# Kernel tuning notes

Hardware: AMD Instinct MI355X
Metric: run time of the kernel (lower is better)

The kernel has to match this reference:

```python
import jax, jax.numpy as jnp
import numpy as np
from jax import lax

B_, L, D, EXPAND, N, R, K = 2, 1024, 1024, 2, 16, 64, 4
ED = EXPAND * D


def setup_inputs() -> dict:
    key = jax.random.key(0)
    ks = jax.random.split(key, 8)
    x = jax.random.normal(ks[0], (B_, L, D), dtype=jnp.float32)
    in_proj_w = jax.random.normal(ks[1], (2 * ED, D), dtype=jnp.float32) * (D ** -0.5)
    in_proj_b = jnp.zeros((2 * ED,), jnp.float32)
    conv_w = jax.random.normal(ks[2], (ED, 1, K), dtype=jnp.float32) * (K ** -0.5)
    conv_b = jnp.zeros((ED,), jnp.float32)
    x_proj_w = jax.random.normal(ks[3], (R + 2 * N, ED), dtype=jnp.float32) * (ED ** -0.5)
    dt_proj_w = jax.random.uniform(ks[4], (ED, R), jnp.float32, -(R ** -0.5), R ** -0.5)
    # inverse-softplus of dt ~ U[log(dt_min), log(dt_max)] (matches torch init)
    dt = jnp.exp(jax.random.uniform(ks[5], (ED,), jnp.float32) * (np.log(0.1) - np.log(0.001)) + np.log(0.001))
    dt_proj_b = dt + jnp.log(-jnp.expm1(-dt))  # softplus^{-1}(dt)
    A_log = jnp.log(jnp.broadcast_to(jnp.arange(1, N + 1, dtype=jnp.float32), (ED, N)))
    D_param = jnp.ones((ED,), jnp.float32)
    out_proj_w = jax.random.normal(ks[6], (D, ED), dtype=jnp.float32) * (ED ** -0.5)
    return {"x": x, "in_proj_w": in_proj_w, "in_proj_b": in_proj_b, "conv_w": conv_w,
            "conv_b": conv_b, "x_proj_w": x_proj_w, "dt_proj_w": dt_proj_w,
            "dt_proj_b": dt_proj_b, "A_log": A_log, "D_param": D_param,
            "out_proj_w": out_proj_w}


def _mamba_fwd(x, in_proj_w, in_proj_b, conv_w, conv_b, x_proj_w, dt_proj_w,
               dt_proj_b, A_log, D_param, out_proj_w):
    xz = x @ in_proj_w.T + in_proj_b                       # (B, L, 2*ED)
    xc, z = jnp.split(xz, 2, axis=-1)                      # (B, L, ED) each
    # causal depthwise conv over time (pad left K-1, valid)
    xc = xc.transpose(0, 2, 1)                             # (B, ED, L)
    xc = lax.conv_general_dilated(xc, conv_w, window_strides=(1,),
                                  padding=[(K - 1, 0)], feature_group_count=ED)
    xc = xc + conv_b[None, :, None]
    xc = jax.nn.silu(xc.transpose(0, 2, 1))                # (B, L, ED)
    # SSM params
    A = -jnp.exp(A_log)                                    # (ED, N)
    dbc = xc @ x_proj_w.T                                  # (B, L, R+2N)
    dt, Bmat, Cmat = jnp.split(dbc, [R, R + N], axis=-1)
    dt = jax.nn.softplus(dt @ dt_proj_w.T + dt_proj_b)     # (B, L, ED)
    dA = jnp.exp(dt[..., None] * A)                        # (B, L, ED, N)
    dBx = (dt * xc)[..., None] * Bmat[:, :, None, :]       # (B, L, ED, N)
    # parallel scan: h_t = dA_t * h_{t-1} + dBx_t
    def combine(e1, e2):
        a1, b1 = e1
        a2, b2 = e2
        return a1 * a2, a2 * b1 + b2
    _, hs = lax.associative_scan(combine, (dA, dBx), axis=1)  # (B, L, ED, N)
    y = jnp.einsum('bln,blen->ble', Cmat, hs) + D_param * xc  # (B, L, ED)
    out = (y * jax.nn.silu(z)) @ out_proj_w.T                 # (B, L, D)
    return out


def reference(x, in_proj_w, in_proj_b, conv_w, conv_b, x_proj_w, dt_proj_w,
              dt_proj_b, A_log, D_param, out_proj_w):
    return _mamba_fwd(x, in_proj_w, in_proj_b, conv_w, conv_b, x_proj_w,
                      dt_proj_w, dt_proj_b, A_log, D_param, out_proj_w)
```

## Files before the change

### kernel.cpp

```cpp
#include <hip/hip_runtime.h>
#include <cstddef>


#define BL   2048
#define DIM  1024
#define ED   2048
#define NST  16
#define RLOW 64
#define CH   64
#define LC   16
#define SK   16
#define DBCN 196608

typedef __attribute__((ext_vector_type(4))) float   f32x4;
typedef __attribute__((ext_vector_type(8))) __bf16  bf16x8;
typedef __attribute__((ext_vector_type(8))) unsigned short us8;

__device__ __forceinline__ float silu_(float x) {
  return x / (1.f + __expf(-x));
}

__device__ __forceinline__ unsigned short f2b(float x) {
  union { float f; unsigned int u; } v; v.f = x;
  unsigned int r = v.u + 0x7FFFu + ((v.u >> 16) & 1u);
  return (unsigned short)(r >> 16);
}

__device__ __forceinline__ float b2f(unsigned short u) {
  union { unsigned int i; float f; } v; v.i = (unsigned int)u << 16; return v.f;
}

__device__ __forceinline__ f32x4 mfma_bf16(us8 a, us8 b, f32x4 c) {
  return __builtin_amdgcn_mfma_f32_16x16x32_bf16(
      __builtin_bit_cast(bf16x8, a), __builtin_bit_cast(bf16x8, b), c, 0, 0, 0);
}

#define GLOAD_LDS16(gaddr, laddr)                                              \
  __builtin_amdgcn_global_load_lds(                                            \
      (const __attribute__((address_space(1))) unsigned int*)(gaddr),          \
      (__attribute__((address_space(3))) unsigned int*)(laddr), 16, 0, 0)

template <int BM, int BN, bool OBF>
__global__ __launch_bounds__(256) void gemm_bf16(
    const unsigned short* __restrict__ A,
    const unsigned short* __restrict__ W,
    const float* __restrict__ bias,
    void* __restrict__ Cp, int ldc, int Nout, int Kloop, int lda, int sstride)
{
  constexpr int BK     = 64;
  constexpr int FM     = BM / 32;
  constexpr int FN     = BN / 32;
  constexpr int NLA    = BM / 32;
  constexpr int NLW    = BN / 32;
  constexpr int ABYTES = BM * BK * 2;
  constexpr int WBYTES = BN * BK * 2;
  __shared__ char smem[2 * (ABYTES + WBYTES)];

  const int tid  = threadIdx.x;
  const int w    = tid >> 6;
  const int lane = tid & 63;
  const int wr   = w >> 1, wc = w & 1;
  const int bm   = blockIdx.x * BM;
  const int bn   = blockIdx.y * BN;
  const int kb   = blockIdx.z * Kloop;

  f32x4 acc[FM][FN];
#pragma unroll
  for (int m = 0; m < FM; ++m)
#pragma unroll
    for (int n = 0; n < FN; ++n) acc[m][n] = (f32x4){0.f, 0.f, 0.f, 0.f};

  const int srow = ((tid >> 7) << 4) | (tid & 15);
  const int kch  = (tid >> 4) & 7;
  const int wofs = (tid >> 6) * 1024;

  const unsigned short* Ag = A + (size_t)(bm + srow) * lda + kb + kch * 8;
  const unsigned short* Wg = W + (size_t)(bn + srow) * lda + kb + kch * 8;

#define STAGE(cur, k0)                                                         \
  {                                                                            \
    char* ab = smem + (cur) * (ABYTES + WBYTES);                               \
    char* wb = ab + ABYTES;                                                    \
    _Pragma("unroll")                                                          \
    for (int j = 0; j < NLA; ++j)                                              \
      GLOAD_LDS16(Ag + (size_t)(j * 32) * lda + (k0), ab + j * 4096 + wofs);   \
    _Pragma("unroll")                                                          \
    for (int j = 0; j < NLW; ++j)                                              \
      GLOAD_LDS16(Wg + (size_t)(j * 32) * lda + (k0), wb + j * 4096 + wofs);   \
  }

  STAGE(0, 0);
  int cur = 0;
  const int NT = Kloop / BK;
  for (int t = 0; t < NT; ++t) {
    __syncthreads();
    if (t + 1 < NT) STAGE(cur ^ 1, (t + 1) * BK);

    const char* ab = smem + cur * (ABYTES + WBYTES);
    const char* wb = ab + ABYTES;
    us8 af[FM][2], wf[FN][2];
#pragma unroll
    for (int m = 0; m < FM; ++m)
#pragma unroll
      for (int h = 0; h < 2; ++h)
        af[m][h] = *(const us8*)(ab + (wr * FM + m) * 2048 + h * 1024 + lane * 16);
#pragma unroll
    for (int n = 0; n < FN; ++n)
#pragma unroll
      for (int h = 0; h < 2; ++h)
        wf[n][h] = *(const us8*)(wb + (wc * FN + n) * 2048 + h * 1024 + lane * 16);
#pragma unroll
    for (int h = 0; h < 2; ++h)
#pragma unroll
      for (int m = 0; m < FM; ++m)
#pragma unroll
        for (int n = 0; n < FN; ++n)
          acc[m][n] = mfma_bf16(af[m][h], wf[n][h], acc[m][n]);
    cur ^= 1;
  }
#undef STAGE

  const int rbase = (lane >> 4) * 4;
  float* Cf = (float*)Cp + (size_t)blockIdx.z * sstride;
#pragma unroll
  for (int m = 0; m < FM; ++m) {
#pragma unroll
    for (int n = 0; n < FN; ++n) {
      const int col = bn + wc * (BN / 2) + n * 16 + (lane & 15);
      if (col < Nout) {
        const float bv = bias ? bias[col] : 0.f;
#pragma unroll
        for (int r = 0; r < 4; ++r) {
          const int row = bm + wr * (BM / 2) + m * 16 + rbase + r;
          const float v = acc[m][n][r] + bv;
          if (OBF) ((unsigned short*)Cp)[(size_t)row * ldc + col] = f2b(v);
          else     Cf[(size_t)row * ldc + col] = v;
        }
      }
    }
  }
}

__global__ __launch_bounds__(256) void reduce_dbc_k(
    const float* __restrict__ par, float* __restrict__ dbc)
{
  const int i = blockIdx.x * 256 + threadIdx.x;
  float4 s = ((const float4*)par)[i];
#pragma unroll
  for (int sk = 1; sk < SK; ++sk) {
    float4 v = ((const float4*)(par + (size_t)sk * DBCN))[i];
    s.x += v.x; s.y += v.y; s.z += v.z; s.w += v.w;
  }
  ((float4*)dbc)[i] = s;
}

__global__ __launch_bounds__(256) void reduce_out_k(
    const float* __restrict__ par, float* __restrict__ out)
{
  const int i = blockIdx.x * 256 + threadIdx.x;
  float4 a = ((const float4*)par)[i];
  float4 b = ((const float4*)(par + 2097152))[i];
  a.x += b.x; a.y += b.y; a.z += b.z; a.w += b.w;
  ((float4*)out)[i] = a;
}

template <int ACT>
__global__ __launch_bounds__(256) void gemm_nt(
    const float* __restrict__ A, int lda,
    const float* __restrict__ W, int ldw,
    const float* __restrict__ bias,
    float* __restrict__ C, int ldc,
    int N, int K)
{
  __shared__ float As[16][64];
  __shared__ float Ws[16][64];
  const int tid = threadIdx.x;
  const int bm = blockIdx.x * 64;
  const int bn = blockIdx.y * 64;
  const int tx = tid & 15;
  const int ty = tid >> 4;
  const int srow = tid >> 2;
  const int scg  = (tid & 3) * 4;

  float acc[4][4] = {};
  const float* Aptr = A + (size_t)(bm + srow) * lda + scg;
  const bool   wok  = (bn + srow) < N;
  const float* Wptr = W + (size_t)(bn + srow) * ldw + scg;

  for (int k0 = 0; k0 < K; k0 += 16) {
    float4 av = *(const float4*)(Aptr + k0);
    float4 wv = make_float4(0.f, 0.f, 0.f, 0.f);
    if (wok) wv = *(const float4*)(Wptr + k0);
    __syncthreads();
    As[scg + 0][srow] = av.x; As[scg + 1][srow] = av.y;
    As[scg + 2][srow] = av.z; As[scg + 3][srow] = av.w;
    Ws[scg + 0][srow] = wv.x; Ws[scg + 1][srow] = wv.y;
    Ws[scg + 2][srow] = wv.z; Ws[scg + 3][srow] = wv.w;
    __syncthreads();
#pragma unroll
    for (int k = 0; k < 16; ++k) {
      float4 a4 = *(const float4*)&As[k][ty * 4];
      float4 w4 = *(const float4*)&Ws[k][tx * 4];
      float a_[4] = {a4.x, a4.y, a4.z, a4.w};
      float w_[4] = {w4.x, w4.y, w4.z, w4.w};
#pragma unroll
      for (int i = 0; i < 4; ++i)
#pragma unroll
        for (int j = 0; j < 4; ++j)
          acc[i][j] += a_[i] * w_[j];
    }
  }

#pragma unroll
  for (int i = 0; i < 4; ++i) {
    const int row = bm + ty * 4 + i;
#pragma unroll
    for (int j = 0; j < 4; ++j) {
      const int col = bn + tx * 4 + j;
      if (col < N) {
        float v = acc[i][j];
        if (bias) v += bias[col];
        if (ACT == 1) v = (v > 20.f) ? v : log1pf(__expf(v));
        C[(size_t)row * ldc + col] = v;
      }
    }
  }
}

__global__ __launch_bounds__(256) void cvt_all_k(
    const float* __restrict__ x, const float* __restrict__ inw,
    const float* __restrict__ ow, const float* __restrict__ xpw,
    unsigned short* __restrict__ xb, unsigned short* __restrict__ iwb,
    unsigned short* __restrict__ owb, unsigned short* __restrict__ xpwb)
{
  const int i = blockIdx.x * 256 + threadIdx.x;
  const float* src; unsigned short* dst; int j;
  if (i < 524288)       { src = x;   dst = xb;  j = i; }
  else if (i < 1572864) { src = inw; dst = iwb; j = i - 524288; }
  else if (i < 2097152) { src = ow;  dst = owb; j = i - 1572864; }
  else {
    j = i - 2097152;
    const int idx = j * 4;
    ushort4 o = {0, 0, 0, 0};
    if ((idx >> 11) < 96) {
      float4 v = *(const float4*)(xpw + idx);
      o.x = f2b(v.x); o.y = f2b(v.y); o.z = f2b(v.z); o.w = f2b(v.w);
    }
    *(ushort4*)(xpwb + idx) = o;
    return;
  }
  float4 v = ((const float4*)src)[j];
  ushort4 o;
  o.x = f2b(v.x); o.y = f2b(v.y); o.z = f2b(v.z); o.w = f2b(v.w);
  ((ushort4*)dst)[j] = o;
}

__global__ __launch_bounds__(256) void conv_silu_k(
    const unsigned short* __restrict__ xzb, const float* __restrict__ cw,
    const float* __restrict__ cb, unsigned short* __restrict__ xcb)
{
  const int idx = blockIdx.x * 256 + threadIdx.x;
  const int row = idx >> 9;
  const int e   = (idx & 511) * 4;
  const int l   = row & 1023;
  const unsigned short* base = xzb + (size_t)(row - l) * (2 * ED) + e;

  float4 cbv = *(const float4*)(cb + e);
  float a0 = cbv.x, a1 = cbv.y, a2 = cbv.z, a3 = cbv.w;
#pragma unroll
  for (int k = 0; k < 4; ++k) {
    const int ls = l - 3 + k;
    if (ls >= 0) {
      ushort4 u = *(const ushort4*)(base + (size_t)ls * (2 * ED));
      a0 += cw[(size_t)(e + 0) * 4 + k] * b2f(u.x);
      a1 += cw[(size_t)(e + 1) * 4 + k] * b2f(u.y);
      a2 += cw[(size_t)(e + 2) * 4 + k] * b2f(u.z);
      a3 += cw[(size_t)(e + 3) * 4 + k] * b2f(u.w);
    }
  }
  ushort4 o;
  o.x = f2b(silu_(a0)); o.y = f2b(silu_(a1));
  o.z = f2b(silu_(a2)); o.w = f2b(silu_(a3));
  *(ushort4*)(xcb + (size_t)row * ED + e) = o;
}

__global__ __launch_bounds__(256, 4) void scan_phase1(
    const float* __restrict__ dt, const unsigned short* __restrict__ xcb,
    const float* __restrict__ dbc, const float* __restrict__ A_log,
    float* __restrict__ aprod_o, float* __restrict__ bfin_o)
{
  const int g  = blockIdx.x * 256 + threadIdx.x;
  const int e  = g & (ED - 1);
  const int bc = g >> 11;
  const int b  = bc >> 6;
  const int c  = bc & (CH - 1);
  const size_t rowbase = (size_t)b * 1024 + (size_t)c * LC;

  __shared__ float4 sB[LC][4];
  if (threadIdx.x < LC * 4) {
    const int row = threadIdx.x >> 2, q = threadIdx.x & 3;
    sB[row][q] = ((const float4*)(dbc + (rowbase + row) * 96 + RLOW))[q];
  }
  __syncthreads();

  float Aen[NST];
  {
    const float4* Ap = (const float4*)(A_log + (size_t)e * NST);
#pragma unroll
    for (int q = 0; q < 4; ++q) {
      float4 v = Ap[q];
      Aen[q*4+0] = -__expf(v.x); Aen[q*4+1] = -__expf(v.y);
      Aen[q*4+2] = -__expf(v.z); Aen[q*4+3] = -__expf(v.w);
    }
  }

  float dtv[LC], dxv[LC];
#pragma unroll
  for (int i = 0; i < LC; ++i) dtv[i] = dt[(rowbase + i) * ED + e];
#pragma unroll
  for (int i = 0; i < LC; ++i)
    dxv[i] = dtv[i] * b2f(xcb[(rowbase + i) * ED + e]);

  float h[NST], ap[NST];
#pragma unroll
  for (int n = 0; n < NST; ++n) { h[n] = 0.f; ap[n] = 1.f; }

  for (int i = 0; i < LC; ++i) {
    float Bv[NST];
#pragma unroll
    for (int q = 0; q < 4; ++q) {
      float4 v = sB[i][q];
      Bv[q*4+0]=v.x; Bv[q*4+1]=v.y; Bv[q*4+2]=v.z; Bv[q*4+3]=v.w;
    }
#pragma unroll
    for (int n = 0; n < NST; ++n) {
      const float dA = __expf(dtv[i] * Aen[n]);
      ap[n] *= dA;
      h[n] = fmaf(dA, h[n], dxv[i] * Bv[n]);
    }
  }

  const size_t obase = ((size_t)(b * ED + e) * CH + c) * NST;
  float4* ao = (float4*)(aprod_o + obase);
  float4* bo = (float4*)(bfin_o + obase);
#pragma unroll
  for (int q = 0; q < 4; ++q) {
    ao[q] = make_float4(ap[q*4+0], ap[q*4+1], ap[q*4+2], ap[q*4+3]);
    bo[q] = make_float4(h[q*4+0],  h[q*4+1],  h[q*4+2],  h[q*4+3]);
  }
}

__global__ __launch_bounds__(256) void scan_phase2(
    const float* __restrict__ aprod, float* __restrict__ bfin)
{
  const int be   = blockIdx.x * 4 + (threadIdx.x >> 6);
  const int lane = threadIdx.x & 63;
  const size_t base = (size_t)be * CH * NST;

  float Aa[NST], Bb[NST];
  {
    const float4* ap4 = (const float4*)(aprod + base);
    const float4* bp4 = (const float4*)(bfin + base);
#pragma unroll
    for (int q = 0; q < 4; ++q) {
      float4 v = ap4[lane * 4 + q];
      Aa[q*4+0]=v.x; Aa[q*4+1]=v.y; Aa[q*4+2]=v.z; Aa[q*4+3]=v.w;
      float4 w = bp4[lane * 4 + q];
      Bb[q*4+0]=w.x; Bb[q*4+1]=w.y; Bb[q*4+2]=w.z; Bb[q*4+3]=w.w;
    }
  }

#pragma unroll
  for (int d = 1; d < 64; d <<= 1) {
#pragma unroll
    for (int r = 0; r < NST; ++r) {
      const float aP = __shfl_up(Aa[r], d);
      const float bP = __shfl_up(Bb[r], d);
      if (lane >= d) {
        Bb[r] = fmaf(Aa[r], bP, Bb[r]);
        Aa[r] *= aP;
      }
    }
  }

#pragma unroll
  for (int r = 0; r < NST; ++r) {
    const float hs = __shfl_up(Bb[r], 1);
    Bb[r] = (lane == 0) ? 0.f : hs;
  }

  float4* ob4 = (float4*)(bfin + base);
#pragma unroll
  for (int q = 0; q < 4; ++q)
    ob4[lane * 4 + q] = make_float4(Bb[q*4+0], Bb[q*4+1], Bb[q*4+2], Bb[q*4+3]);
}

__global__ __launch_bounds__(256, 4) void scan_phase3(
    const float* __restrict__ dt, const unsigned short* __restrict__ xcb,
    const float* __restrict__ dbc, const float* __restrict__ A_log,
    const float* __restrict__ Dp, const unsigned short* __restrict__ xzb,
    const float* __restrict__ hst, unsigned short* __restrict__ ygb)
{
  const int g  = blockIdx.x * 256 + threadIdx.x;
  const int e  = g & (ED - 1);
  const int bc = g >> 11;
  const int b  = bc >> 6;
  const int c  = bc & (CH - 1);
  const size_t rowbase = (size_t)b * 1024 + (size_t)c * LC;

  __shared__ float4 sBC[LC][8];
  if (threadIdx.x < LC * 8) {
    const int row = threadIdx.x >> 3, q = threadIdx.x & 7;
    sBC[row][q] = ((const float4*)(dbc + (rowbase + row) * 96 + RLOW))[q];
  }
  __syncthreads();

  float Aen[NST];
  {
    const float4* Ap = (const float4*)(A_log + (size_t)e * NST);
#pragma unroll
    for (int q = 0; q < 4; ++q) {
      float4 v = Ap[q];
      Aen[q*4+0] = -__expf(v.x); Aen[q*4+1] = -__expf(v.y);
      Aen[q*4+2] = -__expf(v.z); Aen[q*4+3] = -__expf(v.w);
    }
  }

  float dtv[LC], xcv[LC];
#pragma unroll
  for (int i = 0; i < LC; ++i) dtv[i] = dt[(rowbase + i) * ED + e];
#pragma unroll
  for (int i = 0; i < LC; ++i) xcv[i] = b2f(xcb[(rowbase + i) * ED + e]);

  float h[NST];
  {
    const float4* Hp = (const float4*)(hst + ((size_t)(b * ED + e) * CH + c) * NST);
#pragma unroll
    for (int q = 0; q < 4; ++q) {
      float4 v = Hp[q];
      h[q*4+0]=v.x; h[q*4+1]=v.y; h[q*4+2]=v.z; h[q*4+3]=v.w;
    }
  }

  const float De = Dp[e];
  for (int i = 0; i < LC; ++i) {
    const size_t rr = rowbase + i;
    float Bv[NST], Cv[NST];
#pragma unroll
    for (int q = 0; q < 4; ++q) {
      float4 v = sBC[i][q];
      Bv[q*4+0]=v.x; Bv[q*4+1]=v.y; Bv[q*4+2]=v.z; Bv[q*4+3]=v.w;
      float4 w = sBC[i][q + 4];
      Cv[q*4+0]=w.x; Cv[q*4+1]=w.y; Cv[q*4+2]=w.z; Cv[q*4+3]=w.w;
    }
    const float dx = dtv[i] * xcv[i];
    float y = 0.f;
#pragma unroll
    for (int n = 0; n < NST; ++n) {
      const float dA = __expf(dtv[i] * Aen[n]);
      h[n] = fmaf(dA, h[n], dx * Bv[n]);
      y = fmaf(Cv[n], h[n], y);
    }
    y = fmaf(De, xcv[i], y);
    const float zf = b2f(xzb[rr * (2 * ED) + ED + e]);
    ygb[rr * ED + e] = f2b(y * silu_(zf));
  }
}

extern "C" void kernel_launch(void* const* d_in, const int* in_sizes, int n_in,
                              void* d_out, int out_size, void* d_ws, size_t ws_size,
                              hipStream_t stream) {
  const float* x         = (const float*)d_in[0];
  const float* in_w      = (const float*)d_in[1];
  const float* in_b      = (const float*)d_in[2];
  const float* conv_w    = (const float*)d_in[3];
  const float* conv_b    = (const float*)d_in[4];
  const float* xproj_w   = (const float*)d_in[5];
  const float* dtproj_w  = (const float*)d_in[6];
  const float* dtproj_b  = (const float*)d_in[7];
  const float* A_log     = (const float*)d_in[8];
  const float* D_param   = (const float*)d_in[9];
  const float* outproj_w = (const float*)d_in[10];
  float* out = (float*)d_out;

  float* ws    = (float*)d_ws;
  float* dbc   = ws;
  float* dtb   = dbc   + 196608;
  float* aprod = dtb   + 4194304;
  float* bfin  = aprod + 4194304;
  float* parx  = bfin  + 4194304;
  unsigned short* xzb  = (unsigned short*)(parx + 3145728);
  unsigned short* xb   = xzb  + 8388608;
  unsigned short* iwb  = xb   + 2097152;
  unsigned short* owb  = iwb  + 4194304;
  unsigned short* xpwb = owb  + 2097152;
  unsigned short* xcb  = xpwb + 262144;
  unsigned short* ygb  = xcb  + 4194304;
  float* paro  = aprod;

  const dim3 blk(256);

  cvt_all_k<<<dim3(2162688 / 256), blk, 0, stream>>>(
      x, in_w, outproj_w, xproj_w, xb, iwb, owb, xpwb);

  gemm_bf16<128, 128, true><<<dim3(BL / 128, 4096 / 128), blk, 0, stream>>>(
      xb, iwb, in_b, xzb, 2 * ED, 2 * ED, DIM, DIM, 0);

  conv_silu_k<<<dim3((BL * (ED / 4)) / 256), blk, 0, stream>>>(
      xzb, conv_w, conv_b, xcb);

  gemm_bf16<128, 128, false><<<dim3(BL / 128, 1, SK), blk, 0, stream>>>(
      xcb, xpwb, nullptr, parx, 96, 96, ED / SK, ED, DBCN);
  reduce_dbc_k<<<dim3(DBCN / 4 / 256), blk, 0, stream>>>(parx, dbc);

  gemm_nt<1><<<dim3(BL / 64, ED / 64), blk, 0, stream>>>(
      dbc, 96, dtproj_w, RLOW, dtproj_b, dtb, ED, ED, RLOW);

  scan_phase1<<<dim3((2 * CH * ED) / 256), blk, 0, stream>>>(
      dtb, xcb, dbc, A_log, aprod, bfin);
  scan_phase2<<<dim3((2 * ED) / 4), blk, 0, stream>>>(aprod, bfin);
  scan_phase3<<<dim3((2 * CH * ED) / 256), blk, 0, stream>>>(
      dtb, xcb, dbc, A_log, D_param, xzb, bfin, ygb);

  gemm_bf16<64, 128, false><<<dim3(BL / 64, 1024 / 128, 2), blk, 0, stream>>>(
      ygb, owb, nullptr, paro, DIM, DIM, ED / 2, ED, 2097152);
  reduce_out_k<<<dim3(2097152 / 4 / 256), blk, 0, stream>>>(paro, out);
}
```

Before: 217.5 us.

## Run dt_proj GEMM on bf16 MFMA and shrink GEMM K-tile to 32

Replaces the fp32 scalar-FMA dt_proj GEMM with the bf16 MFMA GEMM template. The template gains a fused softplus epilogue, and the dbc reduction now also writes a bf16 copy of the low-rank dt slice. dt_proj weights are converted to bf16 in the existing conversion kernel. All MFMA GEMMs are also changed from BK=64 to BK=32 with a new LDS staging layout, which halves the LDS footprint and lets K=64 work, at the cost of more loop iterations and barriers in the large GEMMs. dt is now computed from bf16 inputs, which lowers its precision.

```diff
diff --git a/kernel.cpp b/kernel.cpp
--- a/kernel.cpp
+++ b/kernel.cpp
@@ -40,18 +40,18 @@
       (const __attribute__((address_space(1))) unsigned int*)(gaddr),          \
       (__attribute__((address_space(3))) unsigned int*)(laddr), 16, 0, 0)
 
-template <int BM, int BN, bool OBF>
+template <int BM, int BN, int ACT, bool OBF>
 __global__ __launch_bounds__(256) void gemm_bf16(
     const unsigned short* __restrict__ A,
     const unsigned short* __restrict__ W,
     const float* __restrict__ bias,
     void* __restrict__ Cp, int ldc, int Nout, int Kloop, int lda, int sstride)
 {
-  constexpr int BK     = 64;
+  constexpr int BK     = 32;
   constexpr int FM     = BM / 32;
   constexpr int FN     = BN / 32;
-  constexpr int NLA    = BM / 32;
-  constexpr int NLW    = BN / 32;
+  constexpr int NLA    = BM / 64;
+  constexpr int NLW    = BN / 64;
   constexpr int ABYTES = BM * BK * 2;
   constexpr int WBYTES = BN * BK * 2;
   __shared__ char smem[2 * (ABYTES + WBYTES)];
@@ -70,9 +70,9 @@
 #pragma unroll
     for (int n = 0; n < FN; ++n) acc[m][n] = (f32x4){0.f, 0.f, 0.f, 0.f};
 
-  const int srow = ((tid >> 7) << 4) | (tid & 15);
-  const int kch  = (tid >> 4) & 7;
-  const int wofs = (tid >> 6) * 1024;
+  const int srow = (w << 4) | (lane & 15);
+  const int kch  = lane >> 4;
+  const int wofs = w * 1024;
 
   const unsigned short* Ag = A + (size_t)(bm + srow) * lda + kb + kch * 8;
   const unsigned short* Wg = W + (size_t)(bn + srow) * lda + kb + kch * 8;
@@ -83,10 +83,10 @@
     char* wb = ab + ABYTES;                                                    \
     _Pragma("unroll")                                                          \
     for (int j = 0; j < NLA; ++j)                                              \
-      GLOAD_LDS16(Ag + (size_t)(j * 32) * lda + (k0), ab + j * 4096 + wofs);   \
+      GLOAD_LDS16(Ag + (size_t)(j * 64) * lda + (k0), ab + j * 4096 + wofs);   \
     _Pragma("unroll")                                                          \
     for (int j = 0; j < NLW; ++j)                                              \
-      GLOAD_LDS16(Wg + (size_t)(j * 32) * lda + (k0), wb + j * 4096 + wofs);   \
+      GLOAD_LDS16(Wg + (size_t)(j * 64) * lda + (k0), wb + j * 4096 + wofs);   \
   }
 
   STAGE(0, 0);
@@ -98,24 +98,18 @@
 
     const char* ab = smem + cur * (ABYTES + WBYTES);
     const char* wb = ab + ABYTES;
-    us8 af[FM][2], wf[FN][2];
+    us8 af[FM], wf[FN];
 #pragma unroll
     for (int m = 0; m < FM; ++m)
-#pragma unroll
-      for (int h = 0; h < 2; ++h)
-        af[m][h] = *(const us8*)(ab + (wr * FM + m) * 2048 + h * 1024 + lane * 16);
+      af[m] = *(const us8*)(ab + (wr * FM + m) * 1024 + lane * 16);
 #pragma unroll
     for (int n = 0; n < FN; ++n)
-#pragma unroll
-      for (int h = 0; h < 2; ++h)
-        wf[n][h] = *(const us8*)(wb + (wc * FN + n) * 2048 + h * 1024 + lane * 16);
-#pragma unroll
-    for (int h = 0; h < 2; ++h)
-#pragma unroll
-      for (int m = 0; m < FM; ++m)
-#pragma unroll
-        for (int n = 0; n < FN; ++n)
-          acc[m][n] = mfma_bf16(af[m][h], wf[n][h], acc[m][n]);
+      wf[n] = *(const us8*)(wb + (wc * FN + n) * 1024 + lane * 16);
+#pragma unroll
+    for (int m = 0; m < FM; ++m)
+#pragma unroll
+      for (int n = 0; n < FN; ++n)
+        acc[m][n] = mfma_bf16(af[m], wf[n], acc[m][n]);
     cur ^= 1;
   }
 #undef STAGE
@@ -132,7 +126,8 @@
 #pragma unroll
         for (int r = 0; r < 4; ++r) {
           const int row = bm + wr * (BM / 2) + m * 16 + rbase + r;
-          const float v = acc[m][n][r] + bv;
+          float v = acc[m][n][r] + bv;
+          if (ACT == 1) v = (v > 20.f) ? v : log1pf(__expf(v));
           if (OBF) ((unsigned short*)Cp)[(size_t)row * ldc + col] = f2b(v);
           else     Cf[(size_t)row * ldc + col] = v;
         }
@@ -142,7 +137,8 @@
 }
 
 __global__ __launch_bounds__(256) void reduce_dbc_k(
-    const float* __restrict__ par, float* __restrict__ dbc)
+    const float* __restrict__ par, float* __restrict__ dbc,
+    unsigned short* __restrict__ dtA)
 {
   const int i = blockIdx.x * 256 + threadIdx.x;
   float4 s = ((const float4*)par)[i];
@@ -152,6 +148,12 @@
     s.x += v.x; s.y += v.y; s.z += v.z; s.w += v.w;
   }
   ((float4*)dbc)[i] = s;
+  const int row = i / 24, c4 = i % 24;
+  if (c4 < 16) {
+    ushort4 o;
+    o.x = f2b(s.x); o.y = f2b(s.y); o.z = f2b(s.z); o.w = f2b(s.w);
+    ((ushort4*)(dtA + (size_t)row * 64))[c4] = o;
+  }
 }
 
 __global__ __launch_bounds__(256) void reduce_out_k(
@@ -164,81 +166,20 @@
   ((float4*)out)[i] = a;
 }
 
-template <int ACT>
-__global__ __launch_bounds__(256) void gemm_nt(
-    const float* __restrict__ A, int lda,
-    const float* __restrict__ W, int ldw,
-    const float* __restrict__ bias,
-    float* __restrict__ C, int ldc,
-    int N, int K)
-{
-  __shared__ float As[16][64];
-  __shared__ float Ws[16][64];
-  const int tid = threadIdx.x;
-  const int bm = blockIdx.x * 64;
-  const int bn = blockIdx.y * 64;
-  const int tx = tid & 15;
-  const int ty = tid >> 4;
-  const int srow = tid >> 2;
-  const int scg  = (tid & 3) * 4;
-
-  float acc[4][4] = {};
-  const float* Aptr = A + (size_t)(bm + srow) * lda + scg;
-  const bool   wok  = (bn + srow) < N;
-  const float* Wptr = W + (size_t)(bn + srow) * ldw + scg;
-
-  for (int k0 = 0; k0 < K; k0 += 16) {
-    float4 av = *(const float4*)(Aptr + k0);
-    float4 wv = make_float4(0.f, 0.f, 0.f, 0.f);
-    if (wok) wv = *(const float4*)(Wptr + k0);
-    __syncthreads();
-    As[scg + 0][srow] = av.x; As[scg + 1][srow] = av.y;
-    As[scg + 2][srow] = av.z; As[scg + 3][srow] = av.w;
-    Ws[scg + 0][srow] = wv.x; Ws[scg + 1][srow] = wv.y;
-    Ws[scg + 2][srow] = wv.z; Ws[scg + 3][srow] = wv.w;
-    __syncthreads();
-#pragma unroll
-    for (int k = 0; k < 16; ++k) {
-      float4 a4 = *(const float4*)&As[k][ty * 4];
-      float4 w4 = *(const float4*)&Ws[k][tx * 4];
-      float a_[4] = {a4.x, a4.y, a4.z, a4.w};
-      float w_[4] = {w4.x, w4.y, w4.z, w4.w};
-#pragma unroll
-      for (int i = 0; i < 4; ++i)
-#pragma unroll
-        for (int j = 0; j < 4; ++j)
-          acc[i][j] += a_[i] * w_[j];
-    }
-  }
-
-#pragma unroll
-  for (int i = 0; i < 4; ++i) {
-    const int row = bm + ty * 4 + i;
-#pragma unroll
-    for (int j = 0; j < 4; ++j) {
-      const int col = bn + tx * 4 + j;
-      if (col < N) {
-        float v = acc[i][j];
-        if (bias) v += bias[col];
-        if (ACT == 1) v = (v > 20.f) ? v : log1pf(__expf(v));
-        C[(size_t)row * ldc + col] = v;
-      }
-    }
-  }
-}
-
 __global__ __launch_bounds__(256) void cvt_all_k(
     const float* __restrict__ x, const float* __restrict__ inw,
     const float* __restrict__ ow, const float* __restrict__ xpw,
+    const float* __restrict__ dtw,
     unsigned short* __restrict__ xb, unsigned short* __restrict__ iwb,
-    unsigned short* __restrict__ owb, unsigned short* __restrict__ xpwb)
+    unsigned short* __restrict__ owb, unsigned short* __restrict__ xpwb,
+    unsigned short* __restrict__ dtwb)
 {
   const int i = blockIdx.x * 256 + threadIdx.x;
   const float* src; unsigned short* dst; int j;
   if (i < 524288)       { src = x;   dst = xb;  j = i; }
   else if (i < 1572864) { src = inw; dst = iwb; j = i - 524288; }
   else if (i < 2097152) { src = ow;  dst = owb; j = i - 1572864; }
-  else {
+  else if (i < 2162688) {
     j = i - 2097152;
     const int idx = j * 4;
     ushort4 o = {0, 0, 0, 0};
@@ -248,7 +189,7 @@
     }
     *(ushort4*)(xpwb + idx) = o;
     return;
-  }
+  } else                { src = dtw; dst = dtwb; j = i - 2162688; }
   float4 v = ((const float4*)src)[j];
   ushort4 o;
   o.x = f2b(v.x); o.y = f2b(v.y); o.z = f2b(v.z); o.w = f2b(v.w);
@@ -496,25 +437,27 @@
   unsigned short* xpwb = owb  + 2097152;
   unsigned short* xcb  = xpwb + 262144;
   unsigned short* ygb  = xcb  + 4194304;
+  unsigned short* dtA  = ygb  + 4194304;
+  unsigned short* dtwb = dtA  + 131072;
   float* paro  = aprod;
 
   const dim3 blk(256);
 
-  cvt_all_k<<<dim3(2162688 / 256), blk, 0, stream>>>(
-      x, in_w, outproj_w, xproj_w, xb, iwb, owb, xpwb);
-
-  gemm_bf16<128, 128, true><<<dim3(BL / 128, 4096 / 128), blk, 0, stream>>>(
+  cvt_all_k<<<dim3(2195456 / 256), blk, 0, stream>>>(
+      x, in_w, outproj_w, xproj_w, dtproj_w, xb, iwb, owb, xpwb, dtwb);
+
+  gemm_bf16<128, 128, 0, true><<<dim3(BL / 128, 4096 / 128), blk, 0, stream>>>(
       xb, iwb, in_b, xzb, 2 * ED, 2 * ED, DIM, DIM, 0);
 
   conv_silu_k<<<dim3((BL * (ED / 4)) / 256), blk, 0, stream>>>(
       xzb, conv_w, conv_b, xcb);
 
-  gemm_bf16<128, 128, false><<<dim3(BL / 128, 1, SK), blk, 0, stream>>>(
+  gemm_bf16<128, 128, 0, false><<<dim3(BL / 128, 1, SK), blk, 0, stream>>>(
       xcb, xpwb, nullptr, parx, 96, 96, ED / SK, ED, DBCN);
-  reduce_dbc_k<<<dim3(DBCN / 4 / 256), blk, 0, stream>>>(parx, dbc);
-
-  gemm_nt<1><<<dim3(BL / 64, ED / 64), blk, 0, stream>>>(
-      dbc, 96, dtproj_w, RLOW, dtproj_b, dtb, ED, ED, RLOW);
+  reduce_dbc_k<<<dim3(DBCN / 4 / 256), blk, 0, stream>>>(parx, dbc, dtA);
+
+  gemm_bf16<128, 128, 1, false><<<dim3(BL / 128, ED / 128), blk, 0, stream>>>(
+      dtA, dtwb, dtproj_b, dtb, ED, ED, RLOW, RLOW, 0);
 
   scan_phase1<<<dim3((2 * CH * ED) / 256), blk, 0, stream>>>(
       dtb, xcb, dbc, A_log, aprod, bfin);
@@ -522,7 +465,7 @@
   scan_phase3<<<dim3((2 * CH * ED) / 256), blk, 0, stream>>>(
       dtb, xcb, dbc, A_log, D_param, xzb, bfin, ygb);
 
-  gemm_bf16<64, 128, false><<<dim3(BL / 64, 1024 / 128, 2), blk, 0, stream>>>(
+  gemm_bf16<64, 128, 0, false><<<dim3(BL / 64, 1024 / 128, 2), blk, 0, stream>>>(
       ygb, owb, nullptr, paro, DIM, DIM, ED / 2, ED, 2097152);
   reduce_out_k<<<dim3(2097152 / 4 / 256), blk, 0, stream>>>(paro, out);
 }
```

New measurement: 306.9 us. 1.41x slower.
